# Kernel optimization log

Measured on AMD Instinct MI355X. Metric: run time of the kernel, lower is better.

Reference implementation:

```python
import jax, jax.numpy as jnp
import numpy as np

H, E, D, S, B = 16, 1024, 64, 2048, 4  # heads, emb, head_size, seq_len, batch

def setup_inputs() -> dict:
    key = jax.random.key(0)
    ks = jax.random.split(key, 9)
    sc_e = 1.0 / np.sqrt(E)
    sc_hd = 1.0 / np.sqrt(H * D)
    return {
        "x":  jax.random.normal(ks[0], (B, S, E), dtype=jnp.float32),
        # per-head q/k/v projection weights, stacked: [H, E, D]
        "Wq": jax.random.uniform(ks[1], (H, E, D), jnp.float32, -sc_e, sc_e),
        "Wk": jax.random.uniform(ks[2], (H, E, D), jnp.float32, -sc_e, sc_e),
        "Wv": jax.random.uniform(ks[3], (H, E, D), jnp.float32, -sc_e, sc_e),
        "bq": jax.random.uniform(ks[4], (H, D), jnp.float32, -sc_e, sc_e),
        "bk": jax.random.uniform(ks[5], (H, D), jnp.float32, -sc_e, sc_e),
        "bv": jax.random.uniform(ks[6], (H, D), jnp.float32, -sc_e, sc_e),
        # output projection: Linear(H*D -> E)
        "Wo": jax.random.uniform(ks[7], (H * D, E), jnp.float32, -sc_hd, sc_hd),
        "bo": jax.random.uniform(ks[8], (E,), jnp.float32, -sc_hd, sc_hd),
    }

def reference(x, Wq, Wk, Wv, bq, bk, bv, Wo, bo):
    b, s, e = x.shape
    # batched per-head projections: [B, H, S, D]
    q = jnp.einsum("bse,hed->bhsd", x, Wq) + bq[None, :, None, :]
    k = jnp.einsum("bse,hed->bhsd", x, Wk) + bk[None, :, None, :]
    v = jnp.einsum("bse,hed->bhsd", x, Wv) + bv[None, :, None, :]
    scale = 1.0 / jnp.sqrt(jnp.asarray(q.shape[-1], q.dtype))
    scores = jnp.einsum("bhqd,bhkd->bhqk", q, k) * scale  # [B,H,S,S]
    causal = jnp.tril(jnp.ones((s, s), dtype=bool))
    scores = jnp.where(causal[None, None], scores, jnp.asarray(-jnp.inf, scores.dtype))
    attn = jax.nn.softmax(scores, axis=-1)
    heads = jnp.einsum("bhqk,bhkd->bhqd", attn, v)  # [B,H,S,D]
    concat = heads.transpose(0, 2, 1, 3).reshape(b, s, -1)  # [B,S,H*D]
    return concat @ Wo + bo  # dropout is identity at inference
```

## Files before the change

kernel.cpp:

```cpp
#include <hip/hip_runtime.h>
#include <hip/hip_bf16.h>

#define H_ 16
#define E_ 1024
#define D_ 64
#define S_ 2048
#define B_ 4
#define M_ (B_ * S_)

typedef __bf16 bf16_t;
typedef __bf16 bf16x8 __attribute__((ext_vector_type(8)));
typedef __bf16 bf16x4 __attribute__((ext_vector_type(4)));
typedef float f32x4 __attribute__((ext_vector_type(4)));

typedef __attribute__((address_space(1))) unsigned int gu32;
typedef __attribute__((address_space(3))) unsigned int lu32;

__device__ __forceinline__ f32x4 mfma16(bf16x8 a, bf16x8 b, f32x4 c) {
  return __builtin_amdgcn_mfma_f32_16x16x32_bf16(a, b, c, 0, 0, 0);
}
__device__ __forceinline__ void gl2lds16(const bf16_t* g, bf16_t* l) {
  __builtin_amdgcn_global_load_lds((const gu32*)g, (lu32*)l, 16, 0, 0);
}

#define BAR() asm volatile("s_barrier" ::: "memory")

__device__ __forceinline__ int detect_f32(const unsigned short* __restrict__ xu) {
  int lane = threadIdx.x & 63;
  int cnt = 0;
  for (int i = 0; i < 4; ++i) {
    unsigned short v = xu[(lane * 4 + i) * 2];
    cnt += __popcll(__ballot(((v >> 7) & 0xFF) >= 0xC0));
  }
  return cnt > 16;
}

__global__ __launch_bounds__(256) void convert_x(
    const void* __restrict__ src, bf16_t* __restrict__ dst,
    int* __restrict__ flag, long n) {
  const int f32 = detect_f32((const unsigned short*)src);
  if (blockIdx.x == 0 && threadIdx.x == 0) { flag[0] = f32; flag[1] = 0; }
  long i = ((long)blockIdx.x * 256 + threadIdx.x) * 8;
  if (i >= n) return;
  bf16x8 v;
  if (f32) {
    const float* s = (const float*)src;
    for (int j = 0; j < 8; ++j) v[j] = (bf16_t)s[i + j];
  } else {
    v = *(const bf16x8*)((const bf16_t*)src + i);
  }
  *(bf16x8*)(dst + i) = v;
}

__global__ __launch_bounds__(256) void transpose_k(
    const void* __restrict__ src_, bf16_t* __restrict__ dst,
    const int* __restrict__ flag, int K, int N, long sStride, long dStride) {
  __shared__ __align__(16) bf16_t tile[64][72];
  const int f32 = *flag;
  dst += (long)blockIdx.z * dStride;
  const int tk = blockIdx.x * 64, tn = blockIdx.y * 64;
  const int t = threadIdx.x;
  for (int i = 0; i < 2; ++i) {
    int c = t + i * 256;
    int r = c >> 3, col = (c & 7) * 8;
    if (f32) {
      const float* s = (const float*)src_ + (long)blockIdx.z * sStride;
      const float* p = &s[(long)(tk + r) * N + tn + col];
      for (int j = 0; j < 8; ++j) tile[r][col + j] = (bf16_t)p[j];
    } else {
      const bf16_t* s = (const bf16_t*)src_ + (long)blockIdx.z * sStride;
      *(bf16x8*)&tile[r][col] = *(const bf16x8*)&s[(long)(tk + r) * N + tn + col];
    }
  }
  __syncthreads();
  for (int i = 0; i < 2; ++i) {
    int c = t + i * 256;
    int r = c >> 3, col = (c & 7) * 8;
    bf16x8 v;
    for (int j = 0; j < 8; ++j) v[j] = tile[col + j][r];
    *(bf16x8*)&dst[(long)(tn + r) * K + tk + col] = v;
  }
}

__global__ __launch_bounds__(256) void transpose_qkv(
    const void* __restrict__ s0, const void* __restrict__ s1,
    const void* __restrict__ s2,
    bf16_t* __restrict__ d0, bf16_t* __restrict__ d1, bf16_t* __restrict__ d2,
    const int* __restrict__ flag) {
  __shared__ __align__(16) bf16_t tile[64][72];
  const int f32 = *flag;
  const int which = blockIdx.z >> 4, h = blockIdx.z & 15;
  const void* src_ = which == 0 ? s0 : (which == 1 ? s1 : s2);
  bf16_t* dst = (which == 0 ? d0 : (which == 1 ? d1 : d2)) + (long)h * E_ * D_;
  const long sOff = (long)h * E_ * D_;
  const int tk = blockIdx.x * 64;
  const int t = threadIdx.x;
  for (int i = 0; i < 2; ++i) {
    int c = t + i * 256;
    int r = c >> 3, col = (c & 7) * 8;
    if (f32) {
      const float* s = (const float*)src_ + sOff;
      const float* p = &s[(long)(tk + r) * D_ + col];
      for (int j = 0; j < 8; ++j) tile[r][col + j] = (bf16_t)p[j];
    } else {
      const bf16_t* s = (const bf16_t*)src_ + sOff;
      *(bf16x8*)&tile[r][col] = *(const bf16x8*)&s[(long)(tk + r) * D_ + col];
    }
  }
  __syncthreads();
  for (int i = 0; i < 2; ++i) {
    int c = t + i * 256;
    int r = c >> 3, col = (c & 7) * 8;
    bf16x8 v;
    for (int j = 0; j < 8; ++j) v[j] = tile[col + j][r];
    *(bf16x8*)&dst[(long)r * E_ + tk + col] = v;
  }
}

template <int NBF, int KIND>
__global__ __launch_bounds__(512, 2) void gemm8(
    const bf16_t* __restrict__ A, const bf16_t* __restrict__ Bt,
    const void* __restrict__ bias0, const void* __restrict__ bias1,
    const void* __restrict__ bias2,
    bf16_t* __restrict__ Cq, void* __restrict__ Cout,
    const int* __restrict__ flag) {
  __shared__ __align__(16) bf16_t LA[2 * 256 * 64];
  __shared__ __align__(16) bf16_t LB[2 * NBF * 64 * 64];
  const int t = threadIdx.x;
  const int wave = t >> 6, lane = t & 63;
  const int quad = lane >> 4, l16 = lane & 15;
  const int wm = (wave >> 2) * 128;
  const int wn = (wave & 3) * (NBF * 16);
  constexpr int CPX = (KIND == 0) ? 64 : 32;
  const int bid = blockIdx.x;
  const int wg = (bid & 7) * CPX + (bid >> 3);
  const int m0 = (wg & 31) * 256;
  const int n0 = (wg >> 5) * (NBF * 64);

  f32x4 acc[8][NBF] = {};
  bf16x8 af[4], bfr[NBF];

  const int sr = lane >> 3;
  const int sj = ((lane & 7) ^ sr) << 3;
  auto stA = [&](int u, int tt) {
    bf16_t* l = &LA[(tt & 1) * 16384 + u * 4096 + wave * 512];
    if constexpr (KIND == 0) {
      gl2lds16(&A[(long)(m0 + u * 64 + wave * 8 + sr) * 1024 + (tt & 15) * 64 + sj], l);
    } else {
      int m = m0 + u * 64 + wave * 8 + sr;
      int b = m >> 11, s = m & (S_ - 1);
      gl2lds16(&A[(((long)(b * H_ + (tt & 15))) * S_ + s) * D_ + sj], l);
    }
  };
  auto stB = [&](int u, int tt) {
    bf16_t* l = &LB[(tt & 1) * (NBF * 4096) + u * 4096 + wave * 512];
    gl2lds16(&Bt[(long)(n0 + u * 64 + wave * 8 + sr) * 1024 + (tt & 15) * 64 + sj], l);
  };

  auto rdA = [&](int buf, int i, int kk) {
    int R = wm + i * 16 + l16;
    return *(const bf16x8*)&LA[buf * 16384 + R * 64 + (((kk * 4 + quad) ^ (R & 7)) << 3)];
  };
  auto rdB = [&](int buf, int j, int kk) {
    int R = wn + j * 16 + l16;
    return *(const bf16x8*)&LB[buf * (NBF * 4096) + R * 64 + (((kk * 4 + quad) ^ (R & 7)) << 3)];
  };
  auto quarter = [&](int buf, int kk, int up, bool rb) {
#pragma unroll
    for (int i = 0; i < 4; ++i) af[i] = rdA(buf, up * 4 + i, kk);
    if (rb) {
#pragma unroll
      for (int j = 0; j < NBF; ++j) bfr[j] = rdB(buf, j, kk);
    }
    __builtin_amdgcn_s_setprio(1);
#pragma unroll
    for (int i = 0; i < 4; ++i)
#pragma unroll
      for (int j = 0; j < NBF; ++j)
        acc[up * 4 + i][j] = mfma16(bfr[j], af[i], acc[up * 4 + i][j]);
    __builtin_amdgcn_s_setprio(0);
  };

  stB(0, 0); stB(1, 0);
  if constexpr (NBF == 3) stB(2, 0);
  stA(0, 0); stA(1, 0); stA(2, 0); stA(3, 0);
  stB(0, 1);

#pragma unroll 1
  for (int it = 0; it < 8; ++it) {
    const int T1 = 2 * it + 1, T2 = 2 * it + 2, T3 = 2 * it + 3;
    stB(1, T1);
    if constexpr (NBF == 3) stB(2, T1);
    if constexpr (NBF == 3) asm volatile("s_waitcnt vmcnt(3)" ::: "memory");
    else                    asm volatile("s_waitcnt vmcnt(2)" ::: "memory");
    BAR();
    quarter(0, 0, 0, true);
    BAR();
    stA(0, T1); stA(1, T1);
    BAR();
    quarter(0, 0, 1, false);
    BAR();
    stA(2, T1); stA(3, T1);
    BAR();
    quarter(0, 1, 0, true);
    BAR();
    stB(0, T2);
    BAR();
    quarter(0, 1, 1, false);
    BAR();
    stB(1, T2);
    if constexpr (NBF == 3) stB(2, T2);
    if constexpr (NBF == 3) asm volatile("s_waitcnt vmcnt(3)" ::: "memory");
    else                    asm volatile("s_waitcnt vmcnt(2)" ::: "memory");
    BAR();
    quarter(1, 0, 0, true);
    BAR();
    stA(0, T2); stA(1, T2);
    BAR();
    quarter(1, 0, 1, false);
    BAR();
    stA(2, T2); stA(3, T2);
    BAR();
    quarter(1, 1, 0, true);
    BAR();
    stB(0, T3);
    BAR();
    quarter(1, 1, 1, false);
    BAR();
  }

  const int f32io = flag[0];
  if constexpr (KIND == 0) {
#pragma unroll
    for (int i = 0; i < 8; ++i) {
      const int m = m0 + wm + i * 16 + l16;
      const int b = m >> 11, s = m & (S_ - 1);
#pragma unroll
      for (int j = 0; j < NBF; ++j) {
        const int n = n0 + wn + j * 16 + quad * 4;
        const int which = n >> 10, nin = n & 1023;
        const int h = nin >> 6, d = nin & 63;
        const void* bp = which == 0 ? bias0 : (which == 1 ? bias1 : bias2);
        bf16x4 o;
#pragma unroll
        for (int r = 0; r < 4; ++r) {
          float bv = f32io ? ((const float*)bp)[nin + r]
                           : (float)((const bf16_t*)bp)[nin + r];
          o[r] = (bf16_t)(acc[i][j][r] + bv);
        }
        *(bf16x4*)&Cq[(long)which * (B_ * H_ * S_ * D_) +
                      (((long)(b * H_ + h)) * S_ + s) * D_ + d] = o;
      }
    }
  } else {
#pragma unroll
    for (int i = 0; i < 8; ++i) {
      const long m = m0 + wm + i * 16 + l16;
#pragma unroll
      for (int j = 0; j < NBF; ++j) {
        const int n = n0 + wn + j * 16 + quad * 4;
        if (f32io) {
          f32x4 o;
#pragma unroll
          for (int r = 0; r < 4; ++r)
            o[r] = acc[i][j][r] + ((const float*)bias0)[n + r];
          *(f32x4*)&((float*)Cout)[m * 1024 + n] = o;
        } else {
          bf16x4 o;
#pragma unroll
          for (int r = 0; r < 4; ++r)
            o[r] = (bf16_t)(acc[i][j][r] + (float)((const bf16_t*)bias0)[n + r]);
          *(bf16x4*)&((bf16_t*)Cout)[m * 1024 + n] = o;
        }
      }
    }
  }
}

__global__ __launch_bounds__(256) void attn_k(
    bf16_t* QO,
    const bf16_t* __restrict__ Kg_,
    const bf16_t* __restrict__ Vtg_) {
  __shared__ __align__(16) bf16_t Ks[64 * 64];
  __shared__ __align__(16) bf16_t Vs[64 * 64];
  __shared__ __align__(16) bf16_t Pq[4][32 * 72];
  const int t = threadIdx.x;
  const int wave = t >> 6, lane = t & 63;
  const int quad = lane >> 4, l16 = lane & 15;
  const int bid = blockIdx.x;
  const int qb = 15 - (bid >> 6);
  const int bh = bid & 63;
  const long base = (long)bh * S_ * D_;
  bf16_t* Qg = QO + base;
  const bf16_t* Kg = Kg_ + base;
  const bf16_t* Vt = Vtg_ + base;
  const int q0 = qb * 128, qrl = wave * 32;
  const int rot = ((lane & 7) - (lane >> 3)) & 7;

  bf16x8 qf[2][2];
  for (int n = 0; n < 2; ++n) {
    long row = q0 + qrl + n * 16 + l16;
    bf16x8 a = *(const bf16x8*)&Qg[row * D_ + quad * 8];
    bf16x8 b = *(const bf16x8*)&Qg[row * D_ + 32 + quad * 8];
    for (int j = 0; j < 8; ++j) {
      a[j] = (bf16_t)((float)a[j] * 0.18033688f);
      b[j] = (bf16_t)((float)b[j] * 0.18033688f);
    }
    qf[n][0] = a; qf[n][1] = b;
  }
  bf16x8 ones;
  for (int j = 0; j < 8; ++j) ones[j] = (bf16_t)1.0f;
  f32x4 o_acc[2][4] = {};
  f32x4 lacc[2] = {};

  const int nkt = 2 * qb + 2;
  for (int kt = 0; kt < nkt; ++kt) {
    __syncthreads();
    for (int i = 0; i < 2; ++i) {
      int c = wave * 2 + i;
      gl2lds16(&Kg[(long)(kt * 64 + c * 8 + (lane >> 3)) * D_ + rot * 8],
               &Ks[c * 512]);
      gl2lds16(&Vt[(long)(c * 8 + (lane >> 3)) * S_ + kt * 64 + rot * 8],
               &Vs[c * 512]);
    }
    __syncthreads();

    if (kt * 64 > q0 + qrl + 31) continue;

    f32x4 sc[2][4];
    for (int mt = 0; mt < 4; ++mt) {
      int krow = mt * 16 + l16;
      bf16x8 kf0 = *(const bf16x8*)&Ks[krow * 64 + (((quad + krow) & 7) << 3)];
      bf16x8 kf1 = *(const bf16x8*)&Ks[krow * 64 + (((quad + 4 + krow) & 7) << 3)];
      for (int n = 0; n < 2; ++n) {
        f32x4 z = {0.f, 0.f, 0.f, 0.f};
        z = mfma16(kf0, qf[n][0], z);
        z = mfma16(kf1, qf[n][1], z);
        sc[n][mt] = z;
      }
    }
    if (kt * 64 + 63 > q0 + qrl) {
      for (int n = 0; n < 2; ++n) {
        int qr = q0 + qrl + n * 16 + l16;
        for (int mt = 0; mt < 4; ++mt)
          for (int r = 0; r < 4; ++r) {
            int kc = kt * 64 + mt * 16 + quad * 4 + r;
            if (kc > qr) sc[n][mt][r] = -1e30f;
          }
      }
    }
    for (int n = 0; n < 2; ++n)
      for (int mt = 0; mt < 4; ++mt) {
        bf16x4 pb;
        for (int r = 0; r < 4; ++r)
          pb[r] = (bf16_t)__builtin_amdgcn_exp2f(sc[n][mt][r]);
        *(bf16x4*)&Pq[wave][(n * 16 + l16) * 72 + mt * 16 + quad * 4] = pb;
      }
    bf16x8 pf[2][2];
    for (int m = 0; m < 2; ++m) {
      pf[m][0] = *(const bf16x8*)&Pq[wave][(m * 16 + l16) * 72 + quad * 8];
      pf[m][1] = *(const bf16x8*)&Pq[wave][(m * 16 + l16) * 72 + 32 + quad * 8];
    }
    for (int m = 0; m < 2; ++m) {
      lacc[m] = mfma16(pf[m][0], ones, lacc[m]);
      lacc[m] = mfma16(pf[m][1], ones, lacc[m]);
    }
    for (int dt = 0; dt < 4; ++dt) {
      int drow = dt * 16 + l16;
      bf16x8 vf0 = *(const bf16x8*)&Vs[drow * 64 + (((quad + drow) & 7) << 3)];
      bf16x8 vf1 = *(const bf16x8*)&Vs[drow * 64 + (((quad + 4 + drow) & 7) << 3)];
      for (int m = 0; m < 2; ++m) {
        o_acc[m][dt] = mfma16(pf[m][0], vf0, o_acc[m][dt]);
        o_acc[m][dt] = mfma16(pf[m][1], vf1, o_acc[m][dt]);
      }
    }
  }
  for (int m = 0; m < 2; ++m)
    for (int r = 0; r < 4; ++r) {
      float inv = 1.0f / lacc[m][r];
      long qg = q0 + qrl + m * 16 + quad * 4 + r;
      for (int dt = 0; dt < 4; ++dt)
        Qg[qg * D_ + dt * 16 + l16] = (bf16_t)(o_acc[m][dt][r] * inv);
    }
}

extern "C" void kernel_launch(void* const* d_in, const int* in_sizes, int n_in,
                              void* d_out, int out_size, void* d_ws, size_t ws_size,
                              hipStream_t stream) {
  (void)in_sizes; (void)n_in; (void)out_size; (void)ws_size;
  const void* x  = d_in[0];
  const void* Wq = d_in[1];
  const void* Wk = d_in[2];
  const void* Wv = d_in[3];
  const void* bq = d_in[4];
  const void* bk = d_in[5];
  const void* bv = d_in[6];
  const void* Wo = d_in[7];
  const void* bo = d_in[8];

  char* base = (char*)d_ws;
  int* flag = (int*)base;
  bf16_t* p = (bf16_t*)(base + 16);
  bf16_t* xb_ = p; p += (size_t)M_ * E_;
  bf16_t* qo_ = p; p += (size_t)B_ * H_ * S_ * D_;
  bf16_t* kb_ = p; p += (size_t)B_ * H_ * S_ * D_;
  bf16_t* vb_ = p; p += (size_t)B_ * H_ * S_ * D_;
  bf16_t* wqt = p; p += (size_t)H_ * D_ * E_;
  bf16_t* wkt = p; p += (size_t)H_ * D_ * E_;
  bf16_t* wvt = p; p += (size_t)H_ * D_ * E_;
  bf16_t* wot = p; p += (size_t)E_ * E_;

  convert_x<<<(M_ * E_) / (256 * 8), 256, 0, stream>>>(x, xb_, flag, (long)M_ * E_);

  transpose_qkv<<<dim3(16, 1, 48), 256, 0, stream>>>(Wq, Wk, Wv, wqt, wkt, wvt, flag);
  transpose_k<<<dim3(16, 16, 1), 256, 0, stream>>>(Wo, wot, flag, E_, E_, 0, 0);

  gemm8<3, 0><<<dim3(512), 512, 0, stream>>>(
      xb_, wqt, bq, bk, bv, qo_, nullptr, flag);

  transpose_k<<<dim3(S_ / 64, 1, B_ * H_), 256, 0, stream>>>(
      vb_, xb_, flag + 1, S_, D_, (long)S_ * D_, (long)S_ * D_);

  attn_k<<<dim3(1024), 256, 0, stream>>>(qo_, kb_, xb_);

  gemm8<2, 1><<<dim3(256), 512, 0, stream>>>(
      qo_, wot, bo, nullptr, nullptr, nullptr, d_out, flag);
}
```

Before: 303.2 us.

## Replace quarter-step GEMM pipeline with whole-tile double-buffered stage/compute loop

Replaces the fine-grained schedule with a simpler one. Before, the projection GEMM main loop interleaved partial A/B tile loads with four compute quarters per buffer, separated by many barriers. Now each iteration issues a full k-tile load into the other LDS buffer, waits once, then runs every MFMA for the current buffer. The aim is to cut barrier count and per-quarter LDS read overhead. The cost is coarser overlap of global-to-LDS traffic with compute, higher register pressure from holding all A/B fragments for both k halves, and one redundant tile load at the end of the loop.

```diff
diff --git a/kernel.cpp b/kernel.cpp
--- a/kernel.cpp
+++ b/kernel.cpp
@@ -138,7 +138,6 @@
   const int n0 = (wg >> 5) * (NBF * 64);
 
   f32x4 acc[8][NBF] = {};
-  bf16x8 af[4], bfr[NBF];
 
   const int sr = lane >> 3;
   const int sj = ((lane & 7) ^ sr) << 3;
@@ -156,6 +155,11 @@
     bf16_t* l = &LB[(tt & 1) * (NBF * 4096) + u * 4096 + wave * 512];
     gl2lds16(&Bt[(long)(n0 + u * 64 + wave * 8 + sr) * 1024 + (tt & 15) * 64 + sj], l);
   };
+  auto stage = [&](int tt) {
+    stB(0, tt); stB(1, tt);
+    if constexpr (NBF == 3) stB(2, tt);
+    stA(0, tt); stA(1, tt); stA(2, tt); stA(3, tt);
+  };
 
   auto rdA = [&](int buf, int i, int kk) {
     int R = wm + i * 16 + l16;
@@ -165,69 +169,46 @@
     int R = wn + j * 16 + l16;
     return *(const bf16x8*)&LB[buf * (NBF * 4096) + R * 64 + (((kk * 4 + quad) ^ (R & 7)) << 3)];
   };
-  auto quarter = [&](int buf, int kk, int up, bool rb) {
-#pragma unroll
-    for (int i = 0; i < 4; ++i) af[i] = rdA(buf, up * 4 + i, kk);
-    if (rb) {
-#pragma unroll
-      for (int j = 0; j < NBF; ++j) bfr[j] = rdB(buf, j, kk);
-    }
+  auto compute = [&](int buf) {
+    bf16x8 a0[8], a1[8], b0[NBF], b1[NBF];
+#pragma unroll
+    for (int j = 0; j < NBF; ++j) b0[j] = rdB(buf, j, 0);
+#pragma unroll
+    for (int i = 0; i < 8; ++i) a0[i] = rdA(buf, i, 0);
+#pragma unroll
+    for (int j = 0; j < NBF; ++j) b1[j] = rdB(buf, j, 1);
+#pragma unroll
+    for (int i = 0; i < 8; ++i) a1[i] = rdA(buf, i, 1);
     __builtin_amdgcn_s_setprio(1);
 #pragma unroll
-    for (int i = 0; i < 4; ++i)
+    for (int i = 0; i < 8; ++i)
 #pragma unroll
       for (int j = 0; j < NBF; ++j)
-        acc[up * 4 + i][j] = mfma16(bfr[j], af[i], acc[up * 4 + i][j]);
+        acc[i][j] = mfma16(b0[j], a0[i], acc[i][j]);
+#pragma unroll
+    for (int i = 0; i < 8; ++i)
+#pragma unroll
+      for (int j = 0; j < NBF; ++j)
+        acc[i][j] = mfma16(b1[j], a1[i], acc[i][j]);
     __builtin_amdgcn_s_setprio(0);
   };
 
-  stB(0, 0); stB(1, 0);
-  if constexpr (NBF == 3) stB(2, 0);
-  stA(0, 0); stA(1, 0); stA(2, 0); stA(3, 0);
-  stB(0, 1);
+  stage(0);
 
 #pragma unroll 1
-  for (int it = 0; it < 8; ++it) {
-    const int T1 = 2 * it + 1, T2 = 2 * it + 2, T3 = 2 * it + 3;
-    stB(1, T1);
-    if constexpr (NBF == 3) stB(2, T1);
-    if constexpr (NBF == 3) asm volatile("s_waitcnt vmcnt(3)" ::: "memory");
-    else                    asm volatile("s_waitcnt vmcnt(2)" ::: "memory");
+  for (int tt = 0; tt < 16; tt += 2) {
+    stage(tt + 1);
+    asm volatile("s_waitcnt vmcnt(%0)" :: "n"(NBF + 4) : "memory");
     BAR();
-    quarter(0, 0, 0, true);
+    compute(0);
     BAR();
-    stA(0, T1); stA(1, T1);
+    stage(tt + 2);
+    asm volatile("s_waitcnt vmcnt(%0)" :: "n"(NBF + 4) : "memory");
     BAR();
-    quarter(0, 0, 1, false);
+    compute(1);
     BAR();
-    stA(2, T1); stA(3, T1);
-    BAR();
-    quarter(0, 1, 0, true);
-    BAR();
-    stB(0, T2);
-    BAR();
-    quarter(0, 1, 1, false);
-    BAR();
-    stB(1, T2);
-    if constexpr (NBF == 3) stB(2, T2);
-    if constexpr (NBF == 3) asm volatile("s_waitcnt vmcnt(3)" ::: "memory");
-    else                    asm volatile("s_waitcnt vmcnt(2)" ::: "memory");
-    BAR();
-    quarter(1, 0, 0, true);
-    BAR();
-    stA(0, T2); stA(1, T2);
-    BAR();
-    quarter(1, 0, 1, false);
-    BAR();
-    stA(2, T2); stA(3, T2);
-    BAR();
-    quarter(1, 1, 0, true);
-    BAR();
-    stB(0, T3);
-    BAR();
-    quarter(1, 1, 1, false);
-    BAR();
-  }
+  }
+  asm volatile("s_waitcnt vmcnt(0)" ::: "memory");
 
   const int f32io = flag[0];
   if constexpr (KIND == 0) {
```

Result: no change. 300.9 us (-0.7%).
